# Kernel optimization log

Hardware: AMD Instinct MI355X
Metric: run time of the kernel (lower is better)

Reference implementation:

```python
import jax, jax.numpy as jnp
import numpy as np
import math

SIZE = 64
SCALE = math.sqrt(SIZE)
EPS = 1e-12  # torch F.normalize default eps

def l2_normalize(x, axis):
    n = jnp.linalg.norm(x, ord=2, axis=axis, keepdims=True)
    return x / jnp.maximum(n, EPS)

def setup_inputs() -> dict:
    key = jax.random.key(0)
    k1, k2, k3 = jax.random.split(key, 3)
    n, l, s, d, v = 8, 2048, 2048, SIZE, SIZE
    return {
        "query": jax.random.normal(k1, (n, l, d), dtype=jnp.float32),
        "key": jax.random.normal(k2, (n, s, d), dtype=jnp.float32),
        "value": jax.random.normal(k3, (n, s, v), dtype=jnp.float32),
        "mask": jnp.ones((n, l, s), dtype=bool),
    }

def reference(query, key, value, mask):
    # rank-3 query path with normalize=True (cosine attention)
    q = l2_normalize(query, 2)
    k = l2_normalize(key, 2)
    score = jnp.einsum('nlk,nsk->nls', q, k) / SCALE
    score = jnp.where(mask, score, -jnp.inf)
    score = jax.nn.softmax(score, axis=2)  # [n, l, s]
    # equivalent to (score.unsqueeze(3) * value.unsqueeze(1)).sum(2)
    output_value = jnp.einsum('nls,nsv->nlv', score, value)
    return (output_value, score)
```

## Files before the change

### kernel.cpp

```cpp
#include <hip/hip_runtime.h>
#include <hip/hip_bf16.h>
#include <math.h>


typedef __bf16 bf16x8 __attribute__((ext_vector_type(8)));
typedef __bf16 bf16x4 __attribute__((ext_vector_type(4)));
typedef float f32x4 __attribute__((ext_vector_type(4)));

#define NB 8
#define LL 2048
#define SS 2048
#define DD 64

__global__ __launch_bounds__(256) void prep_norm(const float* __restrict__ q,
                                                 const float* __restrict__ k,
                                                 __bf16* __restrict__ Qb,
                                                 __bf16* __restrict__ Kb) {
  int w = threadIdx.x >> 6, lane = threadIdx.x & 63;
  int r = blockIdx.x * 4 + w;
  const float* src;
  __bf16* dst;
  float extra;
  if (r < NB * LL) {
    src = q + (size_t)r * DD;
    dst = Qb + (size_t)r * DD;
    extra = 0.125f;
  } else {
    int rk = r - NB * LL;
    src = k + (size_t)rk * DD;
    dst = Kb + (size_t)rk * DD;
    extra = 1.0f;
  }
  float x = src[lane];
  float ss = x * x;
  ss += __shfl_xor(ss, 1);
  ss += __shfl_xor(ss, 2);
  ss += __shfl_xor(ss, 4);
  ss += __shfl_xor(ss, 8);
  ss += __shfl_xor(ss, 16);
  ss += __shfl_xor(ss, 32);
  float nrm = sqrtf(ss);
  float sc = extra / fmaxf(nrm, 1e-12f);
  dst[lane] = (__bf16)(x * sc);
}

__global__ __launch_bounds__(256) void prep_vt(const float* __restrict__ v,
                                               __bf16* __restrict__ Vt) {
  __shared__ __bf16 tile[64][72];
  int n = blockIdx.y;
  int s0 = blockIdx.x * 64;
  int t = threadIdx.x;
#pragma unroll
  for (int it = 0; it < 4; ++it) {
    int idx = t + it * 256;
    int s = idx >> 4, c = idx & 15;
    float4 f = *(const float4*)(v + ((size_t)(n * SS + s0 + s)) * DD + c * 4);
    tile[s][c * 4 + 0] = (__bf16)f.x;
    tile[s][c * 4 + 1] = (__bf16)f.y;
    tile[s][c * 4 + 2] = (__bf16)f.z;
    tile[s][c * 4 + 3] = (__bf16)f.w;
  }
  __syncthreads();
#pragma unroll
  for (int it = 0; it < 4; ++it) {
    int idx = t + it * 256;
    int vv = idx >> 4, c = idx & 15;
    bf16x4 o;
    o[0] = tile[c * 4 + 0][vv];
    o[1] = tile[c * 4 + 1][vv];
    o[2] = tile[c * 4 + 2][vv];
    o[3] = tile[c * 4 + 3][vv];
    *(bf16x4*)(Vt + ((size_t)(n * DD + vv)) * SS + s0 + c * 4) = o;
  }
}

__global__ __launch_bounds__(256, 4) void attn_main(const __bf16* __restrict__ Qb,
                                                    const __bf16* __restrict__ Kb,
                                                    const __bf16* __restrict__ Vt,
                                                    const int* __restrict__ mask,
                                                    float* __restrict__ out_val,
                                                    float* __restrict__ out_score) {
  __shared__ __bf16 e_lds[2][16][72];
  __shared__ float rs_lds[4][16];

  const int n = blockIdx.y;
  const int l0 = blockIdx.x * 16;
  const int t = threadIdx.x;
  const int w = t >> 6;
  const int lane = t & 63;
  const int m16 = lane & 15;
  const int quad = lane >> 4;

  const __bf16* qrow = Qb + ((size_t)(n * LL + l0 + m16)) * DD;
  bf16x8 aq0 = *(const bf16x8*)(qrow + quad * 8);
  bf16x8 aq1 = *(const bf16x8*)(qrow + 32 + quad * 8);

  const __bf16* kbase = Kb + (size_t)n * SS * DD;
  const __bf16* vbase = Vt + (size_t)n * DD * SS;
  const size_t mrow_base = ((size_t)(n * LL + l0)) * SS;

  f32x4 acc_o = {0.f, 0.f, 0.f, 0.f};
  float rsum[4] = {0.f, 0.f, 0.f, 0.f};

  for (int c = 0; c < SS / 64; ++c) {
    const int sc = c * 64;
    const int scol = sc + w * 16 + m16;
    const __bf16* krow = kbase + (size_t)scol * DD;
    bf16x8 b0 = *(const bf16x8*)(krow + quad * 8);
    bf16x8 b1 = *(const bf16x8*)(krow + 32 + quad * 8);
    f32x4 acc = {0.f, 0.f, 0.f, 0.f};
    acc = __builtin_amdgcn_mfma_f32_16x16x32_bf16(aq0, b0, acc, 0, 0, 0);
    acc = __builtin_amdgcn_mfma_f32_16x16x32_bf16(aq1, b1, acc, 0, 0, 0);
#pragma unroll
    for (int r = 0; r < 4; ++r) {
      int row = quad * 4 + r;
      int mk = mask[mrow_base + (size_t)row * SS + scol];
      float e = mk ? __expf(acc[r]) : 0.0f;
      rsum[r] += e;
      e_lds[c & 1][row][w * 16 + m16] = (__bf16)e;
    }
    __syncthreads();
#pragma unroll
    for (int ks = 0; ks < 2; ++ks) {
      bf16x8 ae = *(const bf16x8*)(&e_lds[c & 1][m16][ks * 32 + quad * 8]);
      bf16x8 bv = *(const bf16x8*)(vbase + (size_t)(16 * w + m16) * SS + sc + ks * 32 + quad * 8);
      acc_o = __builtin_amdgcn_mfma_f32_16x16x32_bf16(ae, bv, acc_o, 0, 0, 0);
    }
  }

#pragma unroll
  for (int r = 0; r < 4; ++r) {
    float s = rsum[r];
    s += __shfl_xor(s, 1);
    s += __shfl_xor(s, 2);
    s += __shfl_xor(s, 4);
    s += __shfl_xor(s, 8);
    rsum[r] = s;
  }
  if (m16 == 0) {
#pragma unroll
    for (int r = 0; r < 4; ++r) rs_lds[w][quad * 4 + r] = rsum[r];
  }
  __syncthreads();
  float inv[4];
#pragma unroll
  for (int r = 0; r < 4; ++r) {
    int row = quad * 4 + r;
    float s = rs_lds[0][row] + rs_lds[1][row] + rs_lds[2][row] + rs_lds[3][row];
    inv[r] = 1.0f / s;
  }

#pragma unroll
  for (int r = 0; r < 4; ++r) {
    int row = quad * 4 + r;
    out_val[((size_t)(n * LL + l0 + row)) * DD + 16 * w + m16] = acc_o[r] * inv[r];
  }

  for (int c = 0; c < SS / 64; ++c) {
    const int sc = c * 64;
    const int scol = sc + w * 16 + m16;
    const __bf16* krow = kbase + (size_t)scol * DD;
    bf16x8 b0 = *(const bf16x8*)(krow + quad * 8);
    bf16x8 b1 = *(const bf16x8*)(krow + 32 + quad * 8);
    f32x4 acc = {0.f, 0.f, 0.f, 0.f};
    acc = __builtin_amdgcn_mfma_f32_16x16x32_bf16(aq0, b0, acc, 0, 0, 0);
    acc = __builtin_amdgcn_mfma_f32_16x16x32_bf16(aq1, b1, acc, 0, 0, 0);
#pragma unroll
    for (int r = 0; r < 4; ++r) {
      int row = quad * 4 + r;
      size_t idx = mrow_base + (size_t)row * SS + scol;
      int mk = mask[idx];
      out_score[idx] = mk ? __expf(acc[r]) * inv[r] : 0.0f;
    }
  }
}

extern "C" void kernel_launch(void* const* d_in, const int* in_sizes, int n_in,
                              void* d_out, int out_size, void* d_ws, size_t ws_size,
                              hipStream_t stream) {
  const float* q = (const float*)d_in[0];
  const float* k = (const float*)d_in[1];
  const float* v = (const float*)d_in[2];
  const int* mask = (const int*)d_in[3];

  float* out_val = (float*)d_out;
  float* out_score = out_val + (size_t)NB * LL * DD;

  __bf16* Qb = (__bf16*)d_ws;
  __bf16* Kb = Qb + (size_t)NB * LL * DD;
  __bf16* Vt = Kb + (size_t)NB * SS * DD;

  prep_norm<<<dim3((NB * LL * 2) / 4), dim3(256), 0, stream>>>(q, k, Qb, Kb);
  prep_vt<<<dim3(SS / 64, NB), dim3(256), 0, stream>>>(v, Vt);
  attn_main<<<dim3(LL / 16, NB), dim3(256), 0, stream>>>(Qb, Kb, Vt, mask, out_val, out_score);
}
```

Measured before the change: 329.7 us.

## Stash exp scores in registers to drop second QK pass and mask reread

Uses 512-thread blocks where each wave covers 16 key columns of a 128-wide chunk. The bf16 exp values are kept in a register stash, so the final normalized scores come from the stash rather than from recomputing QK and rereading the mask. Mask loads become vectorized int4 with two-ahead prefetch, score stores become float4, and the two PV halves are reduced through LDS. This removes a second full mask read and the recompute, at the cost of bf16-rounded score outputs and higher register use.

```diff
diff --git a/kernel.cpp b/kernel.cpp
--- a/kernel.cpp
+++ b/kernel.cpp
@@ -74,14 +74,15 @@
   }
 }
 
-__global__ __launch_bounds__(256, 4) void attn_main(const __bf16* __restrict__ Qb,
+__global__ __launch_bounds__(512, 4) void attn_main(const __bf16* __restrict__ Qb,
                                                     const __bf16* __restrict__ Kb,
                                                     const __bf16* __restrict__ Vt,
                                                     const int* __restrict__ mask,
                                                     float* __restrict__ out_val,
                                                     float* __restrict__ out_score) {
-  __shared__ __bf16 e_lds[2][16][72];
-  __shared__ float rs_lds[4][16];
+  __shared__ __bf16 e_lds[2][16][136];
+  __shared__ float rs_lds[8][16];
+  __shared__ float acc_red[4][16][17];
 
   const int n = blockIdx.y;
   const int l0 = blockIdx.x * 16;
@@ -90,88 +91,91 @@
   const int lane = t & 63;
   const int m16 = lane & 15;
   const int quad = lane >> 4;
+  const int vg = w & 3;
+  const int sh = (w >> 2) * 64;
 
   const __bf16* qrow = Qb + ((size_t)(n * LL + l0 + m16)) * DD;
   bf16x8 aq0 = *(const bf16x8*)(qrow + quad * 8);
   bf16x8 aq1 = *(const bf16x8*)(qrow + 32 + quad * 8);
 
   const __bf16* kbase = Kb + (size_t)n * SS * DD;
-  const __bf16* vbase = Vt + (size_t)n * DD * SS;
-  const size_t mrow_base = ((size_t)(n * LL + l0)) * SS;
+  const __bf16* vrow = Vt + ((size_t)(n * DD + vg * 16 + m16)) * SS + sh;
+  const size_t mrow = ((size_t)(n * LL + l0 + m16)) * SS + w * 16 + quad * 4;
 
   f32x4 acc_o = {0.f, 0.f, 0.f, 0.f};
-  float rsum[4] = {0.f, 0.f, 0.f, 0.f};
-
-  for (int c = 0; c < SS / 64; ++c) {
-    const int sc = c * 64;
-    const int scol = sc + w * 16 + m16;
-    const __bf16* krow = kbase + (size_t)scol * DD;
-    bf16x8 b0 = *(const bf16x8*)(krow + quad * 8);
-    bf16x8 b1 = *(const bf16x8*)(krow + 32 + quad * 8);
+  float rsum = 0.f;
+  bf16x4 stash[16];
+  int4 mkb[2];
+  mkb[0] = *(const int4*)(mask + mrow);
+  mkb[1] = *(const int4*)(mask + mrow + 128);
+
+#pragma unroll
+  for (int c = 0; c < 16; ++c) {
+    const int sc = c * 128;
+    const __bf16* krow = kbase + (size_t)(sc + w * 16 + m16) * DD;
+    bf16x8 kb0 = *(const bf16x8*)(krow + quad * 8);
+    bf16x8 kb1 = *(const bf16x8*)(krow + 32 + quad * 8);
+    bf16x8 bv0 = *(const bf16x8*)(vrow + sc + quad * 8);
+    bf16x8 bv1 = *(const bf16x8*)(vrow + sc + 32 + quad * 8);
     f32x4 acc = {0.f, 0.f, 0.f, 0.f};
-    acc = __builtin_amdgcn_mfma_f32_16x16x32_bf16(aq0, b0, acc, 0, 0, 0);
-    acc = __builtin_amdgcn_mfma_f32_16x16x32_bf16(aq1, b1, acc, 0, 0, 0);
+    acc = __builtin_amdgcn_mfma_f32_16x16x32_bf16(kb0, aq0, acc, 0, 0, 0);
+    acc = __builtin_amdgcn_mfma_f32_16x16x32_bf16(kb1, aq1, acc, 0, 0, 0);
+    const int4 mk = mkb[c & 1];
+    if (c + 2 < 16) mkb[c & 1] = *(const int4*)(mask + mrow + (size_t)(c + 2) * 128);
+    float e0 = mk.x ? __expf(acc[0]) : 0.f;
+    float e1 = mk.y ? __expf(acc[1]) : 0.f;
+    float e2 = mk.z ? __expf(acc[2]) : 0.f;
+    float e3 = mk.w ? __expf(acc[3]) : 0.f;
+    rsum += (e0 + e1) + (e2 + e3);
+    bf16x4 sv;
+    sv[0] = (__bf16)e0;
+    sv[1] = (__bf16)e1;
+    sv[2] = (__bf16)e2;
+    sv[3] = (__bf16)e3;
+    stash[c] = sv;
+    *(bf16x4*)(&e_lds[c & 1][m16][w * 16 + quad * 4]) = sv;
+    __syncthreads();
+    bf16x8 ae0 = *(const bf16x8*)(&e_lds[c & 1][m16][sh + quad * 8]);
+    bf16x8 ae1 = *(const bf16x8*)(&e_lds[c & 1][m16][sh + 32 + quad * 8]);
+    acc_o = __builtin_amdgcn_mfma_f32_16x16x32_bf16(ae0, bv0, acc_o, 0, 0, 0);
+    acc_o = __builtin_amdgcn_mfma_f32_16x16x32_bf16(ae1, bv1, acc_o, 0, 0, 0);
+  }
+
+  rsum += __shfl_xor(rsum, 16);
+  rsum += __shfl_xor(rsum, 32);
+  if (quad == 0) rs_lds[w][m16] = rsum;
+  if (w >= 4) {
+#pragma unroll
+    for (int r = 0; r < 4; ++r) acc_red[vg][quad * 4 + r][m16] = acc_o[r];
+  }
+  __syncthreads();
+
+  float tot = 0.f;
+#pragma unroll
+  for (int ww = 0; ww < 8; ++ww) tot += rs_lds[ww][m16];
+  const float inv_s = 1.0f / tot;
+
+  if (w < 4) {
 #pragma unroll
     for (int r = 0; r < 4; ++r) {
-      int row = quad * 4 + r;
-      int mk = mask[mrow_base + (size_t)row * SS + scol];
-      float e = mk ? __expf(acc[r]) : 0.0f;
-      rsum[r] += e;
-      e_lds[c & 1][row][w * 16 + m16] = (__bf16)e;
+      const int row = quad * 4 + r;
+      float tr = 0.f;
+#pragma unroll
+      for (int ww = 0; ww < 8; ++ww) tr += rs_lds[ww][row];
+      const float o = (acc_o[r] + acc_red[vg][row][m16]) / tr;
+      out_val[((size_t)(n * LL + l0 + row)) * DD + vg * 16 + m16] = o;
     }
-    __syncthreads();
-#pragma unroll
-    for (int ks = 0; ks < 2; ++ks) {
-      bf16x8 ae = *(const bf16x8*)(&e_lds[c & 1][m16][ks * 32 + quad * 8]);
-      bf16x8 bv = *(const bf16x8*)(vbase + (size_t)(16 * w + m16) * SS + sc + ks * 32 + quad * 8);
-      acc_o = __builtin_amdgcn_mfma_f32_16x16x32_bf16(ae, bv, acc_o, 0, 0, 0);
-    }
-  }
-
-#pragma unroll
-  for (int r = 0; r < 4; ++r) {
-    float s = rsum[r];
-    s += __shfl_xor(s, 1);
-    s += __shfl_xor(s, 2);
-    s += __shfl_xor(s, 4);
-    s += __shfl_xor(s, 8);
-    rsum[r] = s;
-  }
-  if (m16 == 0) {
-#pragma unroll
-    for (int r = 0; r < 4; ++r) rs_lds[w][quad * 4 + r] = rsum[r];
-  }
-  __syncthreads();
-  float inv[4];
-#pragma unroll
-  for (int r = 0; r < 4; ++r) {
-    int row = quad * 4 + r;
-    float s = rs_lds[0][row] + rs_lds[1][row] + rs_lds[2][row] + rs_lds[3][row];
-    inv[r] = 1.0f / s;
-  }
-
-#pragma unroll
-  for (int r = 0; r < 4; ++r) {
-    int row = quad * 4 + r;
-    out_val[((size_t)(n * LL + l0 + row)) * DD + 16 * w + m16] = acc_o[r] * inv[r];
-  }
-
-  for (int c = 0; c < SS / 64; ++c) {
-    const int sc = c * 64;
-    const int scol = sc + w * 16 + m16;
-    const __bf16* krow = kbase + (size_t)scol * DD;
-    bf16x8 b0 = *(const bf16x8*)(krow + quad * 8);
-    bf16x8 b1 = *(const bf16x8*)(krow + 32 + quad * 8);
-    f32x4 acc = {0.f, 0.f, 0.f, 0.f};
-    acc = __builtin_amdgcn_mfma_f32_16x16x32_bf16(aq0, b0, acc, 0, 0, 0);
-    acc = __builtin_amdgcn_mfma_f32_16x16x32_bf16(aq1, b1, acc, 0, 0, 0);
-#pragma unroll
-    for (int r = 0; r < 4; ++r) {
-      int row = quad * 4 + r;
-      size_t idx = mrow_base + (size_t)row * SS + scol;
-      int mk = mask[idx];
-      out_score[idx] = mk ? __expf(acc[r]) * inv[r] : 0.0f;
-    }
+  }
+
+  float* orow = out_score + mrow;
+#pragma unroll
+  for (int c = 0; c < 16; ++c) {
+    float4 o;
+    o.x = (float)stash[c][0] * inv_s;
+    o.y = (float)stash[c][1] * inv_s;
+    o.z = (float)stash[c][2] * inv_s;
+    o.w = (float)stash[c][3] * inv_s;
+    *(float4*)(orow + (size_t)c * 128) = o;
   }
 }
 
@@ -192,5 +196,5 @@
 
   prep_norm<<<dim3((NB * LL * 2) / 4), dim3(256), 0, stream>>>(q, k, Qb, Kb);
   prep_vt<<<dim3(SS / 64, NB), dim3(256), 0, stream>>>(v, Vt);
-  attn_main<<<dim3(LL / 16, NB), dim3(256), 0, stream>>>(Qb, Kb, Vt, mask, out_val, out_score);
-}
+  attn_main<<<dim3(LL / 16, NB), dim3(512), 0, stream>>>(Qb, Kb, Vt, mask, out_val, out_score);
+}
```

Result: faster. 295.4 us (-10.4%).
